# Kernel tuning notes

Measured on AMD Instinct MI355X. Metric: run time of the kernel, lower is better.

Reference implementation:

```python
import jax, jax.numpy as jnp
import numpy as np

N, E = 3200, 50000
RBF, HID = 16, 128
CUT = 5.0
NS, NV = 32, 16            # multiplicities of 0e and 1o blocks
D = NS + 3 * NV            # 80 = node/message irrep dim
WNUM = NS*NS + NV*NS + NS*NV + NV*NV  # 2304 tensor-product weights per edge
EPS = 1e-8
# path normalization (fully-connected TP, 2 paths per output irrep)
A1 = 1.0 / np.sqrt(2.0 * NS)
A2 = 1.0 / np.sqrt(2.0 * NV)
A3 = 1.0 / np.sqrt(2.0 * NS)
A4 = 1.0 / np.sqrt(2.0 * NV)
ISQ3 = 1.0 / np.sqrt(3.0)


def setup_inputs() -> dict:
    key = jax.random.key(0)
    ks = jax.random.split(key, 24)
    nrm = lambda k, s, sc=1.0: jax.random.normal(k, s, jnp.float32) * sc
    x = nrm(ks[0], (N, D))
    edge_src = jax.random.randint(ks[1], (E,), 0, N)
    edge_dst = jax.random.randint(ks[2], (E,), 0, N)
    dirs = nrm(ks[3], (E, 3))
    unit = dirs / jnp.linalg.norm(dirs, axis=1, keepdims=True)
    # component-normalized SH for l=0,1: [1, sqrt(3)*r_hat]
    edge_sh = jnp.concatenate([jnp.ones((E, 1), jnp.float32), np.sqrt(3.0) * unit], axis=1)
    edge_rbf = nrm(ks[4], (E, RBF))
    edge_len = jax.random.uniform(ks[5], (E,), jnp.float32, 0.1, 6.0)  # some beyond cutoff
    inp = dict(x=x, edge_src=edge_src, edge_dst=edge_dst, edge_sh=edge_sh,
               edge_rbf=edge_rbf, edge_len=edge_len)
    # IrrepNorm affine params
    inp['norm_w'] = jnp.ones((D,), jnp.float32)
    inp['norm_b'] = jnp.zeros((D,), jnp.float32)
    # radial weight MLP (RBF -> HID -> HID -> WNUM)
    inp['mw1'] = nrm(ks[6], (RBF, HID), 1.0/np.sqrt(RBF)); inp['mb1'] = jnp.zeros((HID,), jnp.float32)
    inp['mw2'] = nrm(ks[7], (HID, HID), 1.0/np.sqrt(HID)); inp['mb2'] = jnp.zeros((HID,), jnp.float32)
    inp['mw3'] = nrm(ks[8], (HID, WNUM), 1.0/np.sqrt(HID)); inp['mb3'] = jnp.zeros((WNUM,), jnp.float32)
    # edge gate MLP (RBF -> HID -> 1)
    inp['gw1'] = nrm(ks[9], (RBF, HID), 1.0/np.sqrt(RBF)); inp['gb1'] = jnp.zeros((HID,), jnp.float32)
    inp['gw2'] = nrm(ks[10], (HID, 1), 1.0/np.sqrt(HID)); inp['gb2'] = jnp.zeros((1,), jnp.float32)
    # equivariant linears (e3nn stores N(0,1) weights, normalizes by 1/sqrt(fan_in))
    inp['Ws'] = nrm(ks[11], (NS, NS + NV))   # msg_linear scalar part: 32 -> 32 scalars + 16 gates
    inp['Wv'] = nrm(ks[12], (NV, NV))        # msg_linear vector part
    inp['Us'] = nrm(ks[13], (NS, NS))        # update_linear
    inp['Uv'] = nrm(ks[14], (NV, NV))
    inp['Ss'] = nrm(ks[15], (NS, NS))        # self_linear
    inp['Sv'] = nrm(ks[16], (NV, NV))
    inp['res_scale'] = jnp.float32(0.1)
    return inp


def _irrep_norm(x, w, b):
    s = x[:, :NS]
    v = x[:, NS:].reshape(-1, NV, 3)
    mean = s.mean(axis=1, keepdims=True)
    var = ((s - mean) ** 2).mean(axis=1, keepdims=True)
    s = (s - mean) / jnp.sqrt(var + EPS)
    rms = jnp.sqrt((v ** 2).mean(axis=2, keepdims=True) + EPS)
    v = v / rms
    out = jnp.concatenate([s, v.reshape(-1, 3 * NV)], axis=-1)
    return out * w + b


def reference(x, edge_src, edge_dst, edge_sh, edge_rbf, edge_len,
              norm_w, norm_b, mw1, mb1, mw2, mb2, mw3, mb3,
              gw1, gb1, gw2, gb2, Ws, Wv, Us, Uv, Ss, Sv, res_scale):
    silu = jax.nn.silu
    x_norm = _irrep_norm(x, norm_w, norm_b)                  # [N, 80]
    # radial tensor-product weights per edge
    h = silu(edge_rbf @ mw1 + mb1)
    h = silu(h @ mw2 + mb2)
    tpw = h @ mw3 + mb3                                      # [E, 2304]
    o1 = NS*NS; o2 = o1 + NV*NS; o3 = o2 + NS*NV
    w1 = tpw[:, :o1].reshape(-1, NS, NS)
    w2 = tpw[:, o1:o2].reshape(-1, NV, NS)
    w3 = tpw[:, o2:o3].reshape(-1, NS, NV)
    w4 = tpw[:, o3:].reshape(-1, NV, NV)
    # gather source node features
    xs = x_norm[edge_src, :NS]                               # [E, 32]
    xv = x_norm[edge_src, NS:].reshape(-1, NV, 3)            # [E, 16, 3]
    sh0 = edge_sh[:, 0]                                      # [E]
    sh1 = edge_sh[:, 1:4]                                    # [E, 3]
    # fully-connected TP paths
    msg_s = A1 * jnp.einsum('ei,eio->eo', xs * sh0[:, None], w1)
    inner = jnp.einsum('eim,em->ei', xv, sh1) * ISQ3         # 1o x 1o -> 0e
    msg_s = msg_s + A2 * jnp.einsum('ei,eio->eo', inner, w2)
    msg_v = A3 * jnp.einsum('ei,eio->eo', xs, w3)[:, :, None] * sh1[:, None, :]
    msg_v = msg_v + A4 * jnp.einsum('eim,eio->eom', xv, w4) * sh0[:, None, None]
    m = jnp.concatenate([msg_s, msg_v.reshape(-1, 3 * NV)], axis=-1)  # [E, 80]
    # cutoff envelope and learned edge gate
    cutoff_w = 0.5 * (jnp.cos(jnp.pi * edge_len / CUT) + 1.0) * (edge_len <= CUT).astype(x.dtype)
    gate_w = jax.nn.sigmoid(silu(edge_rbf @ gw1 + gb1) @ gw2 + gb2)   # [E, 1]
    edge_w = cutoff_w[:, None] * gate_w                               # [E, 1]
    m = m * edge_w
    # scatter-add aggregate + normalization
    agg = jax.ops.segment_sum(m, edge_dst, num_segments=N)            # [N, 80]
    den = jax.ops.segment_sum(edge_w, edge_dst, num_segments=N)       # [N, 1]
    agg = agg / jnp.maximum(den, 1e-8)
    # msg_linear -> scalars + gates + gated vectors
    ag_s = agg[:, :NS]
    ag_v = agg[:, NS:].reshape(-1, NV, 3)
    sc = (ag_s @ Ws) / np.sqrt(NS)                                    # [N, 48]
    vc = jnp.einsum('nim,io->nom', ag_v, Wv) / np.sqrt(NV)            # [N, 16, 3]
    s_g = silu(sc[:, :NS])
    gates = jax.nn.sigmoid(sc[:, NS:])
    v_g = vc * gates[:, :, None]
    # update + self interaction
    upd_s = (s_g @ Us) / np.sqrt(NS)
    upd_v = jnp.einsum('nim,io->nom', v_g, Uv) / np.sqrt(NV)
    self_s = (x_norm[:, :NS] @ Ss) / np.sqrt(NS)
    self_v = jnp.einsum('nim,io->nom', x_norm[:, NS:].reshape(-1, NV, 3), Sv) / np.sqrt(NV)
    out = jnp.concatenate([self_s + upd_s, (self_v + upd_v).reshape(-1, 3 * NV)], axis=-1)
    return x + res_scale * out
```

## Files before the change

kernel.cpp:

```cpp
#include <hip/hip_runtime.h>
#include <hip/hip_bf16.h>
#include <math.h>

#define N_NODES 3200
#define E_EDGES 50000
#define RBFN 16
#define HID 128
#define NS 32
#define NV 16
#define DD 80
#define WNUM 2304
#define CUTF 5.0f
#define EPSF 1e-8f

#define A1C 0.125f
#define A2C 0.17677669529663687f
#define A3C 0.125f
#define A4C 0.17677669529663687f
#define A2ISQ 0.10206207261596575f

typedef __attribute__((ext_vector_type(4))) float f32x4;
typedef __attribute__((ext_vector_type(8))) short bf16x8;

__device__ __forceinline__ float sigm(float x) { return 1.0f / (1.0f + __expf(-x)); }
__device__ __forceinline__ float silu_f(float x) { return x * sigm(x); }

__device__ __forceinline__ short bf16r(float x) {
    union { float f; unsigned u; } v; v.f = x;
    unsigned r = (v.u + 0x7fffu + ((v.u >> 16) & 1u)) >> 16;
    return (short)r;
}
__device__ __forceinline__ float b2f(unsigned short s) {
    union { float f; unsigned u; } v; v.u = ((unsigned)s) << 16; return v.f;
}

__global__ void k_hist(const int* __restrict__ edst, int* __restrict__ hist) {
    int e = blockIdx.x * 256 + threadIdx.x;
    if (e < E_EDGES) atomicAdd(&hist[edst[e]], 1);
}

__global__ void k_scan(const int* __restrict__ hist, int* __restrict__ start) {
    __shared__ int part[256];
    int t = threadIdx.x;
    int loc[13];
    int s = 0;
#pragma unroll
    for (int j = 0; j < 13; j++) {
        int idx = t * 13 + j;
        int v = (idx < N_NODES) ? hist[idx] : 0;
        loc[j] = s; s += v;
    }
    part[t] = s;
    __syncthreads();
    for (int off = 1; off < 256; off <<= 1) {
        int v = part[t];
        int add = (t >= off) ? part[t - off] : 0;
        __syncthreads();
        part[t] = v + add;
        __syncthreads();
    }
    int pre = (t == 0) ? 0 : part[t - 1];
#pragma unroll
    for (int j = 0; j < 13; j++) {
        int idx = t * 13 + j;
        if (idx < N_NODES) start[idx] = pre + loc[j];
    }
    if (t == 255) start[N_NODES] = part[255];
}

__global__ void k_scatter(const int* __restrict__ edst, const int* __restrict__ esrc,
                          const float* __restrict__ esh, const int* __restrict__ start,
                          int* __restrict__ cur, int* __restrict__ inv,
                          int* __restrict__ edstp, int* __restrict__ esrcp,
                          float* __restrict__ eshp) {
    int e = blockIdx.x * 256 + threadIdx.x;
    if (e < E_EDGES) {
        int d = edst[e];
        int pos = start[d] + atomicAdd(&cur[d], 1);
        inv[e] = pos;
        edstp[pos] = d;
        esrcp[pos] = esrc[e];
        f32x4 s = *(const f32x4*)(esh + e * 4);
        *(f32x4*)(eshp + pos * 4) = s;
    }
}

__global__ void k_prep0(const float* __restrict__ mw2, __hip_bfloat16* __restrict__ mw2f) {
    __shared__ __hip_bfloat16 st[2048];
    int t = blockIdx.x, tid = threadIdx.x;
    for (int idx = tid; idx < 2048; idx += 256) {
        int k = idx >> 4, c = idx & 15;
        float v = mw2[k * HID + t * 16 + c];
        int kk = k >> 5, q4 = (k >> 3) & 3, j = k & 7;
        st[kk * 512 + (q4 * 16 + c) * 8 + j] = __float2bfloat16(v);
    }
    __syncthreads();
    ((bf16x8*)(mw2f + t * 2048))[tid] = ((const bf16x8*)st)[tid];
}

__global__ __launch_bounds__(256) void k_front(
    const float* __restrict__ rbf, const float* __restrict__ elen,
    const int* __restrict__ inv,
    const float* __restrict__ mw1, const float* __restrict__ mb1,
    const float* __restrict__ gw1, const float* __restrict__ gb1,
    const float* __restrict__ gw2, const float* __restrict__ gb2,
    const float* __restrict__ mb2, const __hip_bfloat16* __restrict__ mw2f,
    const float* __restrict__ mw3, const float* __restrict__ mb3,
    const float* __restrict__ x, const float* __restrict__ nw, const float* __restrict__ nb,
    float* __restrict__ ewg, unsigned short* __restrict__ h2p,
    __hip_bfloat16* __restrict__ mw3f, __hip_bfloat16* __restrict__ biasf,
    float* __restrict__ xn, unsigned short* __restrict__ xnb) {
    __shared__ __align__(16) char smem[16640];
    int b = blockIdx.x, tid = threadIdx.x;
    if (b < 782) {
        __hip_bfloat16* h1l = (__hip_bfloat16*)smem;
        float* gatep = (float*)(smem + 16384);
        int wid = __builtin_amdgcn_readfirstlane(tid >> 6);
        int lane = tid & 63;
        int base = b * 64;
        int eb = base + wid * 16;
        {
            int c0 = lane, c1 = 64 + lane;
            float t0[16], t1[16], g0[16], g1[16];
            float b0 = mb1[c0], b1 = mb1[c1], gb0v = gb1[c0], gb1v = gb1[c1];
#pragma unroll
            for (int e = 0; e < 16; e++) { t0[e] = b0; t1[e] = b1; g0[e] = gb0v; g1[e] = gb1v; }
#pragma unroll
            for (int r = 0; r < RBFN; r++) {
                float w0 = mw1[r * HID + c0], w1 = mw1[r * HID + c1];
                float v0 = gw1[r * HID + c0], v1 = gw1[r * HID + c1];
#pragma unroll
                for (int e = 0; e < 16; e++) {
                    int ee = eb + e; if (ee >= E_EDGES) ee = E_EDGES - 1;
                    float rv = rbf[ee * RBFN + r];
                    t0[e] += rv * w0; t1[e] += rv * w1;
                    g0[e] += rv * v0; g1[e] += rv * v1;
                }
            }
            float q0 = gw2[c0], q1 = gw2[c1];
            float gb2v = gb2[0];
#pragma unroll
            for (int e = 0; e < 16; e++) {
                int le = wid * 16 + e;
                h1l[le * 128 + c0] = __float2bfloat16(silu_f(t0[e]));
                h1l[le * 128 + c1] = __float2bfloat16(silu_f(t1[e]));
                float p = silu_f(g0[e]) * q0 + silu_f(g1[e]) * q1;
                p += __shfl_xor(p, 1);  p += __shfl_xor(p, 2);  p += __shfl_xor(p, 4);
                p += __shfl_xor(p, 8);  p += __shfl_xor(p, 16); p += __shfl_xor(p, 32);
                if (lane == 0) gatep[le] = p + gb2v;
            }
        }
        __syncthreads();
        if (lane < 16) {
            int ee = eb + lane;
            if (ee < E_EDGES) {
                float len = elen[ee];
                float cut = (len <= CUTF) ? 0.5f * (cosf(3.14159265358979f * len / CUTF) + 1.0f) : 0.f;
                ewg[inv[ee]] = cut * sigm(gatep[wid * 16 + lane]);
            }
        }
        {
            int q4 = lane >> 4, l15 = lane & 15;
            int le = wid * 16 + l15;
            bf16x8 af[4];
#pragma unroll
            for (int kk = 0; kk < 4; kk++)
                af[kk] = *(const bf16x8*)(h1l + le * 128 + kk * 32 + q4 * 8);
            int pos4[4];
#pragma unroll
            for (int r = 0; r < 4; r++) {
                int ge = base + wid * 16 + q4 * 4 + r;
                pos4[r] = (ge < E_EDGES) ? inv[ge] : -1;
            }
            const f32x4 zf = {0.f, 0.f, 0.f, 0.f};
#pragma unroll
            for (int ct = 0; ct < 8; ct++) {
                f32x4 acc = zf;
#pragma unroll
                for (int kk = 0; kk < 4; kk++) {
                    bf16x8 bw = *(const bf16x8*)(mw2f + (ct * 4 + kk) * 512 + lane * 8);
                    acc = __builtin_amdgcn_mfma_f32_16x16x32_bf16(af[kk], bw, acc, 0, 0, 0);
                }
                float bias = mb2[ct * 16 + l15];
                int c = ct * 16 + l15;
                int f = c >> 3, j = c & 7;
#pragma unroll
                for (int r = 0; r < 4; r++) {
                    int pos = pos4[r];
                    if (pos >= 0)
                        h2p[(pos >> 4) * 2048 + f * 128 + (pos & 15) * 8 + j] =
                            (unsigned short)bf16r(silu_f(acc[r] + bias));
                }
            }
        }
    } else if (b < 927) {
        int b2 = b - 782;
        __hip_bfloat16* st = (__hip_bfloat16*)smem;
        if (b2 < 144) {
            for (int idx = tid; idx < 2048; idx += 256) {
                int k = idx >> 4, c = idx & 15;
                float v = mw3[k * WNUM + b2 * 16 + c];
                int kk = k >> 5, q4 = (k >> 3) & 3, j = k & 7;
                st[kk * 512 + (q4 * 16 + c) * 8 + j] = __float2bfloat16(v);
            }
            __syncthreads();
            ((bf16x8*)(mw3f + b2 * 2048))[tid] = ((const bf16x8*)st)[tid];
        } else {
            for (int idx = tid; idx < 3072; idx += 256) {
                float val;
                if (idx < 1024) {
                    int oh = idx >> 9, l = (idx >> 3) & 63, j = idx & 7;
                    int o = oh * 16 + (l & 15), i = (l >> 4) * 8 + j;
                    val = mb3[i * 32 + o];
                } else if (idx < 2048) {
                    int t = idx - 1024;
                    int oh = t >> 9, l = (t >> 3) & 63, j = t & 7;
                    int o = oh * 16 + (l & 15), i = (l >> 4) * 8 + j;
                    val = (i < 16) ? mb3[1024 + i * 32 + o] : 0.f;
                } else if (idx < 2560) {
                    int t = idx - 2048;
                    int l = t >> 3, j = t & 7;
                    int o = l & 15, i = (l >> 4) * 8 + j;
                    val = mb3[1536 + i * 16 + o];
                } else {
                    int t = idx - 2560;
                    int l = t >> 3, j = t & 7;
                    int o = l & 15, i = (l >> 4) * 8 + j;
                    val = (i < 16) ? mb3[2048 + i * 16 + o] : 0.f;
                }
                biasf[idx] = __float2bfloat16(val);
            }
        }
    } else {
        float* row = (float*)smem;
        int sub = tid >> 6, t = tid & 63;
        int n = (b - 927) * 4 + sub;
        float* rw = row + sub * 80;
        const float* xr = x + n * DD;
        rw[t] = xr[t];
        if (t < 16) rw[64 + t] = xr[64 + t];
        __syncthreads();
        float mean = 0.f;
#pragma unroll
        for (int i = 0; i < NS; i++) mean += rw[i];
        mean *= (1.0f / NS);
        float var = 0.f;
#pragma unroll
        for (int i = 0; i < NS; i++) { float d = rw[i] - mean; var += d * d; }
        var *= (1.0f / NS);
        float inv_ = rsqrtf(var + EPSF);
        if (t < NS) {
            float v = (rw[t] - mean) * inv_ * nw[t] + nb[t];
            xn[n * DD + t] = v;
            xnb[n * DD + t] = (unsigned short)bf16r(v);
        }
        if (t < 48) {
            int j = t / 3;
            float v0 = rw[NS + 3 * j], v1 = rw[NS + 3 * j + 1], v2 = rw[NS + 3 * j + 2];
            float rms = sqrtf((v0 * v0 + v1 * v1 + v2 * v2) * (1.0f / 3.0f) + EPSF);
            float v = rw[NS + t] / rms * nw[NS + t] + nb[NS + t];
            xn[n * DD + NS + t] = v;
            xnb[n * DD + NS + t] = (unsigned short)bf16r(v);
        }
    }
}

__global__ __launch_bounds__(128, 2) void k_msg(
    const unsigned short* __restrict__ xnb, const unsigned short* __restrict__ h2p,
    const float* __restrict__ ewg, const int* __restrict__ edstp,
    const int* __restrict__ esrcp, const float* __restrict__ eshp,
    const __hip_bfloat16* __restrict__ mw3f, const __hip_bfloat16* __restrict__ biasf,
    const int* __restrict__ startp, float* __restrict__ agg, float* __restrict__ agg2,
    float* __restrict__ den) {
    __shared__ __align__(16) char pool[30720];
    unsigned short (*xng)[88]  = (unsigned short(*)[88])(pool);
    unsigned short (*innr)[16] = (unsigned short(*)[16])(pool + 22528);
    float* sh0l = (float*)(pool + 26624);
    int* srcl   = (int*)(pool + 27136);
    int* dstl   = (int*)(pool + 27648);
    float* ewl  = (float*)(pool + 28160);
    float (*sh1l)[4] = (float(*)[4])(pool + 28672);
    float* msgl = (float*)pool;

    const int tid = threadIdx.x;
    const int wid = __builtin_amdgcn_readfirstlane(tid >> 6);
    const int lane = tid & 63;
    const int q4 = lane >> 4;
    const int l15 = lane & 15;
    const int ib = q4 * 8;
    const int grp = blockIdx.x / 5;
    const int slice = blockIdx.x - 5 * grp;
    const int e0 = grp * 128;

    {
        int slot = e0 + tid;
        bool v = slot < E_EDGES;
        dstl[tid] = v ? edstp[slot] : -1;
        srcl[tid] = v ? esrcp[slot] : 0;
        ewl[tid]  = v ? ewg[slot] : 0.f;
        f32x4 s = {0.f, 0.f, 0.f, 0.f};
        if (v) s = *(const f32x4*)(eshp + slot * 4);
        sh0l[tid] = s[0];
        sh1l[tid][0] = s[1]; sh1l[tid][1] = s[2]; sh1l[tid][2] = s[3];
    }
    __syncthreads();
    if (slice < 2) {
        for (int idx = tid; idx < 128 * 4; idx += 128) {
            int e = idx >> 2, q = (idx & 3) * 8;
            *(bf16x8*)&xng[e][q] = *(const bf16x8*)(xnb + srcl[e] * 80 + q);
        }
    } else if (slice < 4) {
        for (int idx = tid; idx < 128 * 7; idx += 128) {
            int e = idx / 7, q = 24 + (idx - e * 7) * 8;
            *(bf16x8*)&xng[e][q] = *(const bf16x8*)(xnb + srcl[e] * 80 + q);
        }
    } else {
        for (int idx = tid; idx < 128 * 10; idx += 128) {
            int e = idx / 10, q = (idx - e * 10) * 8;
            *(bf16x8*)&xng[e][q] = *(const bf16x8*)(xnb + srcl[e] * 80 + q);
        }
    }
    __syncthreads();
    if (slice == 2 || slice == 3) {
        for (int idx = tid; idx < 128 * 16; idx += 128) {
            int e = idx >> 4, i = idx & 15;
            float d = b2f(xng[e][32 + 3 * i]) * sh1l[e][0]
                    + b2f(xng[e][32 + 3 * i + 1]) * sh1l[e][1]
                    + b2f(xng[e][32 + 3 * i + 2]) * sh1l[e][2];
            innr[e][i] = (unsigned short)bf16r(A2ISQ * d);
        }
        __syncthreads();
    }

    int el[4];
#pragma unroll
    for (int et = 0; et < 4; et++) el[et] = wid * 64 + et * 16 + l15;
    const int tbase = (e0 >> 4) + wid * 4;
    bf16x8 hfr[4][4];
#pragma unroll
    for (int et = 0; et < 4; et++) {
        const unsigned short* tp = h2p + (tbase + et) * 2048;
#pragma unroll
        for (int kk = 0; kk < 4; kk++)
            hfr[et][kk] = *(const bf16x8*)(tp + (kk * 4 + q4) * 128 + l15 * 8);
    }
    const f32x4 zf = {0.f, 0.f, 0.f, 0.f};
    const bf16x8* gp = (const bf16x8*)mw3f;
    int cnt = E_EDGES - e0; if (cnt > 128) cnt = 128;

    if (slice < 4) {
        const int h = slice & 1;
        const int ch2 = slice >> 1;
        const int nlo = ch2 * 24, nhi = nlo + 24;
        float f1[4];
        f32x4 msgS[4];
#pragma unroll
        for (int et = 0; et < 4; et++) f1[et] = A1C * sh0l[el[et]];
#pragma unroll
        for (int et = 0; et < 4; et++) {
            bf16x8 pb;
            if (ch2 == 0) {
#pragma unroll
                for (int j = 0; j < 8; j++)
                    pb[j] = bf16r(b2f(xng[el[et]][ib + j]) * f1[et]);
            } else {
#pragma unroll
                for (int j = 0; j < 8; j++)
                    pb[j] = (ib + j < 16) ? (short)innr[el[et]][ib + j] : (short)0;
            }
            bf16x8 ba = *(const bf16x8*)(biasf + (ch2 * 1024 + h * 512) + lane * 8);
            msgS[et] = __builtin_amdgcn_mfma_f32_16x16x32_bf16(ba, pb, zf, 0, 0, 0);
        }
        auto computeS = [&](int n, bf16x8 (&A)[4]) {
            f32x4 acc[4];
#pragma unroll
            for (int et = 0; et < 4; et++) acc[et] = zf;
#pragma unroll
            for (int kk = 0; kk < 4; kk++)
#pragma unroll
                for (int et = 0; et < 4; et++)
                    acc[et] = __builtin_amdgcn_mfma_f32_16x16x32_bf16(
                        A[kk], hfr[et][kk], acc[et], 0, 0, 0);
            float p[4];
            if (n < 32) {
#pragma unroll
                for (int et = 0; et < 4; et++) p[et] = f1[et] * b2f(xng[el[et]][n]);
            } else {
#pragma unroll
                for (int et = 0; et < 4; et++) p[et] = b2f(innr[el[et]][n - 32]);
            }
#pragma unroll
            for (int et = 0; et < 4; et++)
#pragma unroll
                for (int r = 0; r < 4; r++)
                    msgS[et][r] += p[et] * acc[et][r];
        };
        bf16x8 A0[4], A1[4];
        {
            const bf16x8* g = gp + nlo * 512 + h * 256;
#pragma unroll
            for (int f = 0; f < 4; f++) A0[f] = g[f * 64 + lane];
        }
        for (int n = nlo; n < nhi; n += 2) {
            const bf16x8* g1 = gp + (n + 1) * 512 + h * 256;
#pragma unroll
            for (int f = 0; f < 4; f++) A1[f] = g1[f * 64 + lane];
            computeS(n, A0);
            if (n + 2 < nhi) {
                const bf16x8* g2 = gp + (n + 2) * 512 + h * 256;
#pragma unroll
                for (int f = 0; f < 4; f++) A0[f] = g2[f * 64 + lane];
            }
            computeS(n + 1, A1);
        }
        __syncthreads();
#pragma unroll
        for (int et = 0; et < 4; et++) {
            int le = el[et];
            float ew = ewl[le];
#pragma unroll
            for (int r = 0; r < 4; r++)
                msgl[le * 16 + q4 * 4 + r] = msgS[et][r] * ew;
        }
        __syncthreads();
        {
            int nch = (slice == 0) ? 17 : 16;
            int c = lane;
            int r0 = wid * 64;
            int rend = (cnt < r0 + 64) ? cnt : (r0 + 64);
            if (c < nch && r0 < cnt) {
                int cur = dstl[r0];
                float acc = 0.f;
                for (int r = r0; r < rend; r++) {
                    int nd = dstl[r];
                    if (nd != cur) {
                        if (cur >= 0) {
                            bool interior = (startp[cur] >= e0 + r0) && (startp[cur + 1] <= e0 + rend);
                            float* p = (c == 16) ? (den + cur)
                                     : ((slice == 0) ? (agg + cur * 80 + c)
                                     :  (slice == 1) ? (agg + cur * 80 + 16 + c)
                                     :  (slice == 2) ? (agg2 + cur * 32 + c)
                                                     : (agg2 + cur * 32 + 16 + c));
                            if (interior) *p = acc; else atomicAdd(p, acc);
                        }
                        acc = 0.f; cur = nd;
                    }
                    acc += (c == 16) ? ewl[r] : msgl[r * 16 + c];
                }
                if (cur >= 0) {
                    bool interior = (startp[cur] >= e0 + r0) && (startp[cur + 1] <= e0 + rend);
                    float* p = (c == 16) ? (den + cur)
                             : ((slice == 0) ? (agg + cur * 80 + c)
                             :  (slice == 1) ? (agg + cur * 80 + 16 + c)
                             :  (slice == 2) ? (agg2 + cur * 32 + c)
                                             : (agg2 + cur * 32 + 16 + c));
                    if (interior) *p = acc; else atomicAdd(p, acc);
                }
            }
        }
    } else {
        float f4e[4];
#pragma unroll
        for (int et = 0; et < 4; et++) f4e[et] = A4C * sh0l[el[et]];
        f32x4 q3[4];
#pragma unroll
        for (int et = 0; et < 4; et++) {
            bf16x8 xs8;
#pragma unroll
            for (int j = 0; j < 8; j++) xs8[j] = (short)xng[el[et]][ib + j];
            bf16x8 ba3 = *(const bf16x8*)(biasf + 2048 + lane * 8);
            q3[et] = __builtin_amdgcn_mfma_f32_16x16x32_bf16(ba3, xs8, zf, 0, 0, 0);
        }
        for (int n = 48; n < 64; ++n) {
            bf16x8 A[8];
            const bf16x8* g = gp + n * 512;
#pragma unroll
            for (int f = 0; f < 8; f++) A[f] = g[f * 64 + lane];
#pragma unroll
            for (int half = 0; half < 2; half++) {
                f32x4 acc[4];
#pragma unroll
                for (int et = 0; et < 4; et++) acc[et] = zf;
#pragma unroll
                for (int kk = 0; kk < 4; kk++)
#pragma unroll
                    for (int et = 0; et < 4; et++)
                        acc[et] = __builtin_amdgcn_mfma_f32_16x16x32_bf16(
                            A[half * 4 + kk], hfr[et][kk], acc[et], 0, 0, 0);
                int i = 2 * (n - 48) + half;
                float p[4];
#pragma unroll
                for (int et = 0; et < 4; et++) p[et] = b2f(xng[el[et]][i]);
#pragma unroll
                for (int et = 0; et < 4; et++)
#pragma unroll
                    for (int r = 0; r < 4; r++)
                        q3[et][r] += p[et] * acc[et][r];
            }
        }
        f32x4 qv[3][4];
#pragma unroll
        for (int et = 0; et < 4; et++) {
            bf16x8 ba4 = *(const bf16x8*)(biasf + 2560 + lane * 8);
#pragma unroll
            for (int m = 0; m < 3; m++) {
                bf16x8 t8;
#pragma unroll
                for (int j = 0; j < 8; j++) {
                    int i = ib + j;
                    t8[j] = (i < 16) ? (short)xng[el[et]][32 + 3 * i + m] : (short)0;
                }
                qv[m][et] = __builtin_amdgcn_mfma_f32_16x16x32_bf16(ba4, t8, zf, 0, 0, 0);
            }
        }
        for (int n = 64; n < 72; ++n) {
            bf16x8 A[8];
            const bf16x8* g = gp + n * 512;
#pragma unroll
            for (int f = 0; f < 8; f++) A[f] = g[f * 64 + lane];
#pragma unroll
            for (int half = 0; half < 2; half++) {
                f32x4 acc[4];
#pragma unroll
                for (int et = 0; et < 4; et++) acc[et] = zf;
#pragma unroll
                for (int kk = 0; kk < 4; kk++)
#pragma unroll
                    for (int et = 0; et < 4; et++)
                        acc[et] = __builtin_amdgcn_mfma_f32_16x16x32_bf16(
                            A[half * 4 + kk], hfr[et][kk], acc[et], 0, 0, 0);
                int i = 2 * (n - 64) + half;
#pragma unroll
                for (int m = 0; m < 3; m++) {
                    float p[4];
#pragma unroll
                    for (int et = 0; et < 4; et++) p[et] = b2f(xng[el[et]][32 + 3 * i + m]);
#pragma unroll
                    for (int et = 0; et < 4; et++)
#pragma unroll
                        for (int r = 0; r < 4; r++)
                            qv[m][et][r] += p[et] * acc[et][r];
                }
            }
        }
        __syncthreads();
#pragma unroll
        for (int et = 0; et < 4; et++) {
            int le = el[et];
            float ew = ewl[le];
            float s0 = sh1l[le][0], s1 = sh1l[le][1], s2 = sh1l[le][2];
            float b4 = f4e[et];
#pragma unroll
            for (int r = 0; r < 4; r++) {
                int o = q4 * 4 + r;
                float qq = A3C * q3[et][r];
                msgl[le * 48 + o * 3 + 0] = (qq * s0 + b4 * qv[0][et][r]) * ew;
                msgl[le * 48 + o * 3 + 1] = (qq * s1 + b4 * qv[1][et][r]) * ew;
                msgl[le * 48 + o * 3 + 2] = (qq * s2 + b4 * qv[2][et][r]) * ew;
            }
        }
        __syncthreads();
        {
            int c = lane;
            int r0 = wid * 64;
            int rend = (cnt < r0 + 64) ? cnt : (r0 + 64);
            if (c < 48 && r0 < cnt) {
                int cur = dstl[r0];
                float acc = 0.f;
                for (int r = r0; r < rend; r++) {
                    int nd = dstl[r];
                    if (nd != cur) {
                        if (cur >= 0) {
                            bool interior = (startp[cur] >= e0 + r0) && (startp[cur + 1] <= e0 + rend);
                            float* p = agg + cur * 80 + 32 + c;
                            if (interior) *p = acc; else atomicAdd(p, acc);
                        }
                        acc = 0.f; cur = nd;
                    }
                    acc += msgl[r * 48 + c];
                }
                if (cur >= 0) {
                    bool interior = (startp[cur] >= e0 + r0) && (startp[cur + 1] <= e0 + rend);
                    float* p = agg + cur * 80 + 32 + c;
                    if (interior) *p = acc; else atomicAdd(p, acc);
                }
            }
        }
    }
}

__global__ void k_update(
    const float* __restrict__ x, const float* __restrict__ xn,
    const float* __restrict__ agg, const float* __restrict__ agg2,
    const float* __restrict__ den,
    const float* __restrict__ Ws, const float* __restrict__ Wv,
    const float* __restrict__ Us, const float* __restrict__ Uv,
    const float* __restrict__ Ss, const float* __restrict__ Sv,
    const float* __restrict__ rsp, float* __restrict__ out) {
    int n = blockIdx.x, t = threadIdx.x;
    __shared__ float ag[DD];
    __shared__ float xnl[DD];
    __shared__ float sg[NS];
    __shared__ float gt[NV];
    __shared__ float vg[48];
    float idv = 1.0f / fmaxf(den[n], 1e-8f);
    float base = agg[n * DD + t];
    if (t < 32) base += agg2[n * 32 + t];
    ag[t] = base * idv;
    if (t < 16) ag[64 + t] = agg[n * DD + 64 + t] * idv;
    xnl[t] = xn[n * DD + t];
    if (t < 16) xnl[64 + t] = xn[n * DD + 64 + t];
    __syncthreads();
    const float iqs = 0.17677669529663687f;
    const float iqv = 0.25f;
    if (t < 48) {
        float acc = 0.f;
#pragma unroll
        for (int i = 0; i < NS; i++) acc += ag[i] * Ws[i * 48 + t];
        acc *= iqs;
        if (t < NS) sg[t] = silu_f(acc);
        else gt[t - NS] = sigm(acc);
    }
    __syncthreads();
    if (t < 48) {
        int o = t / 3, m = t - 3 * o;
        float acc = 0.f;
#pragma unroll
        for (int i = 0; i < NV; i++) acc += ag[NS + 3 * i + m] * Wv[i * NV + o];
        vg[t] = acc * iqv * gt[o];
    }
    __syncthreads();
    float rs = rsp[0];
    if (t < NS) {
        float us = 0.f, ss = 0.f;
#pragma unroll
        for (int i = 0; i < NS; i++) { us += sg[i] * Us[i * NS + t]; ss += xnl[i] * Ss[i * NS + t]; }
        out[n * DD + t] = x[n * DD + t] + rs * ((ss + us) * iqs);
    }
    if (t < 48) {
        int o = t / 3, m = t - 3 * o;
        float uv = 0.f, sv = 0.f;
#pragma unroll
        for (int i = 0; i < NV; i++) { uv += vg[3 * i + m] * Uv[i * NV + o]; sv += xnl[NS + 3 * i + m] * Sv[i * NV + o]; }
        out[n * DD + NS + t] = x[n * DD + NS + t] + rs * ((sv + uv) * iqv);
    }
}

extern "C" void kernel_launch(void* const* d_in, const int* in_sizes, int n_in,
                              void* d_out, int out_size, void* d_ws, size_t ws_size,
                              hipStream_t stream) {
    (void)in_sizes; (void)n_in; (void)out_size; (void)ws_size;
    const float* x    = (const float*)d_in[0];
    const int*   esrc = (const int*)d_in[1];
    const int*   edst = (const int*)d_in[2];
    const float* esh  = (const float*)d_in[3];
    const float* erbf = (const float*)d_in[4];
    const float* elen = (const float*)d_in[5];
    const float* nw   = (const float*)d_in[6];
    const float* nb   = (const float*)d_in[7];
    const float* mw1  = (const float*)d_in[8];
    const float* mb1  = (const float*)d_in[9];
    const float* mw2  = (const float*)d_in[10];
    const float* mb2  = (const float*)d_in[11];
    const float* mw3  = (const float*)d_in[12];
    const float* mb3  = (const float*)d_in[13];
    const float* gw1  = (const float*)d_in[14];
    const float* gb1  = (const float*)d_in[15];
    const float* gw2  = (const float*)d_in[16];
    const float* gb2  = (const float*)d_in[17];
    const float* Ws   = (const float*)d_in[18];
    const float* Wv   = (const float*)d_in[19];
    const float* Us   = (const float*)d_in[20];
    const float* Uv   = (const float*)d_in[21];
    const float* Ss   = (const float*)d_in[22];
    const float* Sv   = (const float*)d_in[23];
    const float* rsp  = (const float*)d_in[24];
    float* out = (float*)d_out;
    float* ws  = (float*)d_ws;

    float* agg    = ws;
    float* den    = ws + 256000;
    int*   hist   = (int*)(ws + 259200);
    int*   cur    = (int*)(ws + 262400);
    int*   startp = (int*)(ws + 265600);
    int*   inv    = (int*)(ws + 268801);
    float* xn     = ws + 318804;
    float* ewg    = ws + 574804;
    unsigned short* h2p = (unsigned short*)(ws + 624804);
    __hip_bfloat16* mw3f  = (__hip_bfloat16*)(ws + 3827876);
    __hip_bfloat16* biasf = (__hip_bfloat16*)(ws + 3975332);
    __hip_bfloat16* mw2f  = (__hip_bfloat16*)(ws + 3976868);
    float* agg2   = ws + 3985060;
    int* edstp    = (int*)(ws + 4087460);
    int* esrcp    = (int*)(ws + 4137508);
    float* eshp   = ws + 4187556;
    unsigned short* xnb = (unsigned short*)(ws + 4387748);

    hipMemsetAsync(ws, 0, 265600 * sizeof(float), stream);
    hipMemsetAsync(agg2, 0, 102400 * sizeof(float), stream);
    k_hist<<<196, 256, 0, stream>>>(edst, hist);
    k_scan<<<1, 256, 0, stream>>>(hist, startp);
    k_scatter<<<196, 256, 0, stream>>>(edst, esrc, esh, startp, cur,
                                       inv, edstp, esrcp, eshp);
    k_prep0<<<8, 256, 0, stream>>>(mw2, mw2f);
    k_front<<<1727, 256, 0, stream>>>(erbf, elen, inv, mw1, mb1, gw1, gb1, gw2, gb2,
                                      mb2, mw2f, mw3, mb3, x, nw, nb,
                                      ewg, h2p, mw3f, biasf, xn, xnb);
    k_msg<<<1955, 128, 0, stream>>>(xnb, h2p, ewg, edstp, esrcp, eshp,
                                    mw3f, biasf, startp, agg, agg2, den);
    k_update<<<N_NODES, 64, 0, stream>>>(x, xn, agg, agg2, den, Ws, Wv, Us, Uv, Ss, Sv, rsp, out);
}
```

Before: 240.7 us.

## Split heaviest message slice into two blocks and fuse scan with weight prep

The message kernel now uses six slices per 128-edge group instead of five. The former last slice, which covered weight rows 48..63 and gathered all 80 features, is split into a new slice for rows 48..59 and a remaining slice for rows 60..63. The new slice writes its own partial aggregate buffer, agg3, which the update kernel adds back in. The scan and mw2 bf16 prep kernels are merged into one launch, and the two memsets become one over a reorganised workspace. The aim is to balance per-block work and cut launch count, at the cost of an extra aggregate buffer, more atomics and repeated gathers and edge loads.

Result: slower. 252.7 us (+5.0%).

```diff
diff --git a/kernel.cpp b/kernel.cpp
--- a/kernel.cpp
+++ b/kernel.cpp
@@ -39,33 +39,48 @@
     if (e < E_EDGES) atomicAdd(&hist[edst[e]], 1);
 }
 
-__global__ void k_scan(const int* __restrict__ hist, int* __restrict__ start) {
-    __shared__ int part[256];
-    int t = threadIdx.x;
-    int loc[13];
-    int s = 0;
-#pragma unroll
-    for (int j = 0; j < 13; j++) {
-        int idx = t * 13 + j;
-        int v = (idx < N_NODES) ? hist[idx] : 0;
-        loc[j] = s; s += v;
-    }
-    part[t] = s;
-    __syncthreads();
-    for (int off = 1; off < 256; off <<= 1) {
-        int v = part[t];
-        int add = (t >= off) ? part[t - off] : 0;
-        __syncthreads();
-        part[t] = v + add;
-        __syncthreads();
-    }
-    int pre = (t == 0) ? 0 : part[t - 1];
-#pragma unroll
-    for (int j = 0; j < 13; j++) {
-        int idx = t * 13 + j;
-        if (idx < N_NODES) start[idx] = pre + loc[j];
-    }
-    if (t == 255) start[N_NODES] = part[255];
+__global__ void k_scan_prep(const int* __restrict__ hist, int* __restrict__ start,
+                            const float* __restrict__ mw2, __hip_bfloat16* __restrict__ mw2f) {
+    __shared__ __align__(16) char sm[4096];
+    int b = blockIdx.x, t = threadIdx.x;
+    if (b == 0) {
+        int* part = (int*)sm;
+        int loc[13];
+        int s = 0;
+#pragma unroll
+        for (int j = 0; j < 13; j++) {
+            int idx = t * 13 + j;
+            int v = (idx < N_NODES) ? hist[idx] : 0;
+            loc[j] = s; s += v;
+        }
+        part[t] = s;
+        __syncthreads();
+        for (int off = 1; off < 256; off <<= 1) {
+            int v = part[t];
+            int add = (t >= off) ? part[t - off] : 0;
+            __syncthreads();
+            part[t] = v + add;
+            __syncthreads();
+        }
+        int pre = (t == 0) ? 0 : part[t - 1];
+#pragma unroll
+        for (int j = 0; j < 13; j++) {
+            int idx = t * 13 + j;
+            if (idx < N_NODES) start[idx] = pre + loc[j];
+        }
+        if (t == 255) start[N_NODES] = part[255];
+    } else {
+        __hip_bfloat16* st = (__hip_bfloat16*)sm;
+        int tt = b - 1;
+        for (int idx = t; idx < 2048; idx += 256) {
+            int k = idx >> 4, c = idx & 15;
+            float v = mw2[k * HID + tt * 16 + c];
+            int kk = k >> 5, q4 = (k >> 3) & 3, j = k & 7;
+            st[kk * 512 + (q4 * 16 + c) * 8 + j] = __float2bfloat16(v);
+        }
+        __syncthreads();
+        ((bf16x8*)(mw2f + tt * 2048))[t] = ((const bf16x8*)st)[t];
+    }
 }
 
 __global__ void k_scatter(const int* __restrict__ edst, const int* __restrict__ esrc,
@@ -83,19 +98,6 @@
         f32x4 s = *(const f32x4*)(esh + e * 4);
         *(f32x4*)(eshp + pos * 4) = s;
     }
-}
-
-__global__ void k_prep0(const float* __restrict__ mw2, __hip_bfloat16* __restrict__ mw2f) {
-    __shared__ __hip_bfloat16 st[2048];
-    int t = blockIdx.x, tid = threadIdx.x;
-    for (int idx = tid; idx < 2048; idx += 256) {
-        int k = idx >> 4, c = idx & 15;
-        float v = mw2[k * HID + t * 16 + c];
-        int kk = k >> 5, q4 = (k >> 3) & 3, j = k & 7;
-        st[kk * 512 + (q4 * 16 + c) * 8 + j] = __float2bfloat16(v);
-    }
-    __syncthreads();
-    ((bf16x8*)(mw2f + t * 2048))[tid] = ((const bf16x8*)st)[tid];
 }
 
 __global__ __launch_bounds__(256) void k_front(
@@ -271,7 +273,7 @@
     const int* __restrict__ esrcp, const float* __restrict__ eshp,
     const __hip_bfloat16* __restrict__ mw3f, const __hip_bfloat16* __restrict__ biasf,
     const int* __restrict__ startp, float* __restrict__ agg, float* __restrict__ agg2,
-    float* __restrict__ den) {
+    float* __restrict__ agg3, float* __restrict__ den) {
     __shared__ __align__(16) char pool[30720];
     unsigned short (*xng)[88]  = (unsigned short(*)[88])(pool);
     unsigned short (*innr)[16] = (unsigned short(*)[16])(pool + 22528);
@@ -288,8 +290,8 @@
     const int q4 = lane >> 4;
     const int l15 = lane & 15;
     const int ib = q4 * 8;
-    const int grp = blockIdx.x / 5;
-    const int slice = blockIdx.x - 5 * grp;
+    const int grp = blockIdx.x / 6;
+    const int slice = blockIdx.x - 6 * grp;
     const int e0 = grp * 128;
 
     {
@@ -304,19 +306,14 @@
         sh1l[tid][0] = s[1]; sh1l[tid][1] = s[2]; sh1l[tid][2] = s[3];
     }
     __syncthreads();
-    if (slice < 2) {
+    if (slice == 0 || slice == 1 || slice == 4) {
         for (int idx = tid; idx < 128 * 4; idx += 128) {
             int e = idx >> 2, q = (idx & 3) * 8;
             *(bf16x8*)&xng[e][q] = *(const bf16x8*)(xnb + srcl[e] * 80 + q);
         }
-    } else if (slice < 4) {
+    } else {
         for (int idx = tid; idx < 128 * 7; idx += 128) {
             int e = idx / 7, q = 24 + (idx - e * 7) * 8;
-            *(bf16x8*)&xng[e][q] = *(const bf16x8*)(xnb + srcl[e] * 80 + q);
-        }
-    } else {
-        for (int idx = tid; idx < 128 * 10; idx += 128) {
-            int e = idx / 10, q = (idx - e * 10) * 8;
             *(bf16x8*)&xng[e][q] = *(const bf16x8*)(xnb + srcl[e] * 80 + q);
         }
     }
@@ -458,10 +455,7 @@
                 }
             }
         }
-    } else {
-        float f4e[4];
-#pragma unroll
-        for (int et = 0; et < 4; et++) f4e[et] = A4C * sh0l[el[et]];
+    } else if (slice == 4) {
         f32x4 q3[4];
 #pragma unroll
         for (int et = 0; et < 4; et++) {
@@ -471,7 +465,83 @@
             bf16x8 ba3 = *(const bf16x8*)(biasf + 2048 + lane * 8);
             q3[et] = __builtin_amdgcn_mfma_f32_16x16x32_bf16(ba3, xs8, zf, 0, 0, 0);
         }
-        for (int n = 48; n < 64; ++n) {
+        for (int n = 48; n < 60; ++n) {
+            bf16x8 A[8];
+            const bf16x8* g = gp + n * 512;
+#pragma unroll
+            for (int f = 0; f < 8; f++) A[f] = g[f * 64 + lane];
+#pragma unroll
+            for (int half = 0; half < 2; half++) {
+                f32x4 acc[4];
+#pragma unroll
+                for (int et = 0; et < 4; et++) acc[et] = zf;
+#pragma unroll
+                for (int kk = 0; kk < 4; kk++)
+#pragma unroll
+                    for (int et = 0; et < 4; et++)
+                        acc[et] = __builtin_amdgcn_mfma_f32_16x16x32_bf16(
+                            A[half * 4 + kk], hfr[et][kk], acc[et], 0, 0, 0);
+                int i = 2 * (n - 48) + half;
+                float p[4];
+#pragma unroll
+                for (int et = 0; et < 4; et++) p[et] = b2f(xng[el[et]][i]);
+#pragma unroll
+                for (int et = 0; et < 4; et++)
+#pragma unroll
+                    for (int r = 0; r < 4; r++)
+                        q3[et][r] += p[et] * acc[et][r];
+            }
+        }
+        __syncthreads();
+#pragma unroll
+        for (int et = 0; et < 4; et++) {
+            int le = el[et];
+            float ew = ewl[le];
+            float s0 = sh1l[le][0], s1 = sh1l[le][1], s2 = sh1l[le][2];
+#pragma unroll
+            for (int r = 0; r < 4; r++) {
+                int o = q4 * 4 + r;
+                float qq = A3C * q3[et][r] * ew;
+                msgl[le * 48 + o * 3 + 0] = qq * s0;
+                msgl[le * 48 + o * 3 + 1] = qq * s1;
+                msgl[le * 48 + o * 3 + 2] = qq * s2;
+            }
+        }
+        __syncthreads();
+        {
+            int c = lane;
+            int r0 = wid * 64;
+            int rend = (cnt < r0 + 64) ? cnt : (r0 + 64);
+            if (c < 48 && r0 < cnt) {
+                int cur = dstl[r0];
+                float acc = 0.f;
+                for (int r = r0; r < rend; r++) {
+                    int nd = dstl[r];
+                    if (nd != cur) {
+                        if (cur >= 0) {
+                            bool interior = (startp[cur] >= e0 + r0) && (startp[cur + 1] <= e0 + rend);
+                            float* p = agg3 + cur * 48 + c;
+                            if (interior) *p = acc; else atomicAdd(p, acc);
+                        }
+                        acc = 0.f; cur = nd;
+                    }
+                    acc += msgl[r * 48 + c];
+                }
+                if (cur >= 0) {
+                    bool interior = (startp[cur] >= e0 + r0) && (startp[cur + 1] <= e0 + rend);
+                    float* p = agg3 + cur * 48 + c;
+                    if (interior) *p = acc; else atomicAdd(p, acc);
+                }
+            }
+        }
+    } else {
+        float f4e[4];
+#pragma unroll
+        for (int et = 0; et < 4; et++) f4e[et] = A4C * sh0l[el[et]];
+        f32x4 q3[4];
+#pragma unroll
+        for (int et = 0; et < 4; et++) q3[et] = zf;
+        for (int n = 60; n < 64; ++n) {
             bf16x8 A[8];
             const bf16x8* g = gp + n * 512;
 #pragma unroll
@@ -592,7 +662,7 @@
 __global__ void k_update(
     const float* __restrict__ x, const float* __restrict__ xn,
     const float* __restrict__ agg, const float* __restrict__ agg2,
-    const float* __restrict__ den,
+    const float* __restrict__ agg3, const float* __restrict__ den,
     const float* __restrict__ Ws, const float* __restrict__ Wv,
     const float* __restrict__ Us, const float* __restrict__ Uv,
     const float* __restrict__ Ss, const float* __restrict__ Sv,
@@ -606,8 +676,9 @@
     float idv = 1.0f / fmaxf(den[n], 1e-8f);
     float base = agg[n * DD + t];
     if (t < 32) base += agg2[n * 32 + t];
+    else base += agg3[n * 48 + (t - 32)];
     ag[t] = base * idv;
-    if (t < 16) ag[64 + t] = agg[n * DD + 64 + t] * idv;
+    if (t < 16) ag[64 + t] = (agg[n * DD + 64 + t] + agg3[n * 48 + 32 + t]) * idv;
     xnl[t] = xn[n * DD + t];
     if (t < 16) xnl[64 + t] = xn[n * DD + 64 + t];
     __syncthreads();
@@ -680,33 +751,33 @@
 
     float* agg    = ws;
     float* den    = ws + 256000;
-    int*   hist   = (int*)(ws + 259200);
-    int*   cur    = (int*)(ws + 262400);
-    int*   startp = (int*)(ws + 265600);
-    int*   inv    = (int*)(ws + 268801);
-    float* xn     = ws + 318804;
-    float* ewg    = ws + 574804;
-    unsigned short* h2p = (unsigned short*)(ws + 624804);
-    __hip_bfloat16* mw3f  = (__hip_bfloat16*)(ws + 3827876);
-    __hip_bfloat16* biasf = (__hip_bfloat16*)(ws + 3975332);
-    __hip_bfloat16* mw2f  = (__hip_bfloat16*)(ws + 3976868);
-    float* agg2   = ws + 3985060;
-    int* edstp    = (int*)(ws + 4087460);
-    int* esrcp    = (int*)(ws + 4137508);
-    float* eshp   = ws + 4187556;
-    unsigned short* xnb = (unsigned short*)(ws + 4387748);
-
-    hipMemsetAsync(ws, 0, 265600 * sizeof(float), stream);
-    hipMemsetAsync(agg2, 0, 102400 * sizeof(float), stream);
+    float* agg2   = ws + 259200;
+    float* agg3   = ws + 361600;
+    int*   hist   = (int*)(ws + 515200);
+    int*   cur    = (int*)(ws + 518400);
+    int*   startp = (int*)(ws + 521600);
+    int*   inv    = (int*)(ws + 524804);
+    float* xn     = ws + 574804;
+    float* ewg    = ws + 830804;
+    unsigned short* h2p = (unsigned short*)(ws + 880804);
+    __hip_bfloat16* mw3f  = (__hip_bfloat16*)(ws + 4083876);
+    __hip_bfloat16* biasf = (__hip_bfloat16*)(ws + 4231332);
+    __hip_bfloat16* mw2f  = (__hip_bfloat16*)(ws + 4232868);
+    int* edstp    = (int*)(ws + 4241060);
+    int* esrcp    = (int*)(ws + 4291108);
+    float* eshp   = ws + 4341156;
+    unsigned short* xnb = (unsigned short*)(ws + 4541348);
+
+    hipMemsetAsync(ws, 0, 521600 * sizeof(float), stream);
     k_hist<<<196, 256, 0, stream>>>(edst, hist);
-    k_scan<<<1, 256, 0, stream>>>(hist, startp);
+    k_scan_prep<<<9, 256, 0, stream>>>(hist, startp, mw2, mw2f);
     k_scatter<<<196, 256, 0, stream>>>(edst, esrc, esh, startp, cur,
                                        inv, edstp, esrcp, eshp);
-    k_prep0<<<8, 256, 0, stream>>>(mw2, mw2f);
     k_front<<<1727, 256, 0, stream>>>(erbf, elen, inv, mw1, mb1, gw1, gb1, gw2, gb2,
                                       mb2, mw2f, mw3, mb3, x, nw, nb,
                                       ewg, h2p, mw3f, biasf, xn, xnb);
-    k_msg<<<1955, 128, 0, stream>>>(xnb, h2p, ewg, edstp, esrcp, eshp,
-                                    mw3f, biasf, startp, agg, agg2, den);
-    k_update<<<N_NODES, 64, 0, stream>>>(x, xn, agg, agg2, den, Ws, Wv, Us, Uv, Ss, Sv, rsp, out);
-}
+    k_msg<<<2346, 128, 0, stream>>>(xnb, h2p, ewg, edstp, esrcp, eshp,
+                                    mw3f, biasf, startp, agg, agg2, agg3, den);
+    k_update<<<N_NODES, 64, 0, stream>>>(x, xn, agg, agg2, agg3, den,
+                                         Ws, Wv, Us, Uv, Ss, Sv, rsp, out);
+}
```
